# Kernel tuning notes

Hardware: AMD Instinct MI355X
Metric: run time of the kernel (lower is better)

Reference implementation:

```python
import jax, jax.numpy as jnp
import numpy as np

N = 50000   # num nodes
E = 800000  # num edges (avg degree 16)
L = 4       # num_blocks
H = 128     # hidden_dim
CD = 3      # coords_dim
VD = 3      # vel_dim
FD = 16     # node feature dim = node_dim - coords_dim - vel_dim
ED = 16     # edge_dim
DIN = 2 * H + ED + 1  # edge MLP input dim = 273


def setup_inputs() -> dict:
    key = jax.random.key(0)
    ks = jax.random.split(key, 32)
    s = 0.05
    inp = {}
    inp['nodes'] = jax.random.normal(ks[0], (N, CD + VD + FD), jnp.float32)
    # avoid self-loops (start==end) so the coord-diff norm is never exactly 0
    start = jax.random.randint(ks[1], (E,), 0, N)
    off = jax.random.randint(ks[2], (E,), 1, N)
    inp['edge_indices'] = jnp.stack([start, (start + off) % N]).astype(jnp.int64)
    inp['edge_features'] = jax.random.normal(ks[3], (E, ED), jnp.float32)
    # node embedding
    inp['emb_w'] = (jax.random.normal(ks[4], (FD, H)) * s).astype(jnp.float32)
    inp['emb_b'] = jnp.zeros((H,), jnp.float32)
    # per-block params, stacked over L blocks
    def w(k, shape):
        return (jax.random.normal(k, shape) * s).astype(jnp.float32)
    inp['ew1'] = w(ks[5], (L, DIN, H)); inp['eb1'] = jnp.zeros((L, H), jnp.float32)
    inp['ew2'] = w(ks[6], (L, H, H));   inp['eb2'] = jnp.zeros((L, H), jnp.float32)
    inp['cw1'] = w(ks[7], (L, H, H));   inp['cb1'] = jnp.zeros((L, H), jnp.float32)
    inp['cw2'] = w(ks[8], (L, H, CD));  inp['cb2'] = jnp.zeros((L, CD), jnp.float32)
    inp['vw1'] = w(ks[9], (L, H, H));   inp['vb1'] = jnp.zeros((L, H), jnp.float32)
    inp['vw2'] = w(ks[10], (L, H, 1));  inp['vb2'] = jnp.zeros((L, 1), jnp.float32)
    inp['nw1'] = w(ks[11], (L, 2 * H, H)); inp['nb1'] = jnp.zeros((L, H), jnp.float32)
    inp['nw2'] = w(ks[12], (L, H, H));  inp['nb2'] = jnp.zeros((L, H), jnp.float32)
    return inp


def _forward(nodes, edge_features, emb_w, emb_b, ew1, eb1, ew2, eb2,
             cw1, cb1, cw2, cb2, vw1, vb1, vw2, vb2, nw1, nb1, nw2, nb2,
             edge_indices):
    silu = jax.nn.silu
    coords = nodes[:, :CD]
    vels = nodes[:, CD:CD + VD]
    h = nodes[:, CD + VD:] @ emb_w + emb_b  # [N, H]
    start, end = edge_indices[0], edge_indices[1]
    n = coords.shape[0]
    # per-node edge counts for the coordinate mean-aggregation
    cnt = jax.ops.segment_sum(jnp.ones((start.shape[0], 1), coords.dtype),
                              start, num_segments=n)
    cnt = jnp.maximum(cnt, 1.0)
    for l in range(L):
        cd = coords[start] - coords[end]                       # [E, CD]
        nrm = jnp.sqrt(jnp.sum(cd * cd, axis=1, keepdims=True))  # [E, 1]
        x = jnp.concatenate([h[start], h[end], nrm, edge_features], axis=1)
        m = silu(silu(x @ ew1[l] + eb1[l]) @ ew2[l] + eb2[l])  # [E, H]
        # coordinate update: mean-aggregated weighted diffs + velocity term
        ct = cd * (silu(m @ cw1[l] + cb1[l]) @ cw2[l] + cb2[l])
        coords = coords + jax.ops.segment_sum(ct, start, num_segments=n) / cnt
        coords = coords + (silu(h @ vw1[l] + vb1[l]) @ vw2[l] + vb2[l]) * vels
        # node update: sum-aggregated messages
        agg = jax.ops.segment_sum(m, start, num_segments=n)    # [N, H]
        h = h + silu(jnp.concatenate([h, agg], axis=1) @ nw1[l] + nb1[l]) @ nw2[l] + nb2[l]
    return coords  # prediction_type == 'coords'


def reference(nodes, edge_indices, edge_features, emb_w, emb_b,
              ew1, eb1, ew2, eb2, cw1, cb1, cw2, cb2,
              vw1, vb1, vw2, vb2, nw1, nb1, nw2, nb2):
    return _forward(nodes, edge_features, emb_w, emb_b, ew1, eb1, ew2, eb2,
                    cw1, cb1, cw2, cb2, vw1, vb1, vw2, vb2,
                    nw1, nb1, nw2, nb2, edge_indices)
```

## Files before the change

### kernel.cpp

```cpp
#include <hip/hip_runtime.h>

constexpr int NN = 50000;
constexpr int EE = 800000;
constexpr int HH = 128;

typedef __attribute__((ext_vector_type(8))) __bf16 bfv8;
typedef __attribute__((ext_vector_type(4))) float f32x4;
typedef unsigned short u16;

__device__ __forceinline__ u16 f2bf(float x){
  unsigned u = __builtin_bit_cast(unsigned, x);
  u = u + 0x7fffu + ((u >> 16) & 1u);
  return (u16)(u >> 16);
}
__device__ __forceinline__ float fsilu(float x){
  return x * __builtin_amdgcn_rcpf(1.f + __expf(-x));
}

template<int KSTEPS, int CB>
__device__ __forceinline__ void mm_lds(const u16* Arows, const u16* __restrict__ Bp,
                                       const float* __restrict__ bias, int NB, f32x4* acc){
  const int lane = threadIdx.x & 63;
  #pragma unroll
  for (int cb = 0; cb < CB; ++cb){
    int col = cb*16 + (lane & 15);
    float b = (col < NB) ? bias[col] : 0.f;
    acc[cb] = (f32x4){b, b, b, b};
  }
  const int arow = lane & 15;
  const char* abase = (const char*)Arows + arow * 256;
  const int kb = (lane >> 4) * 16;
  const int swz = (arow & 7) << 4;
  const bfv8* __restrict__ bq = (const bfv8*)Bp + lane;
  #pragma unroll
  for (int ks = 0; ks < KSTEPS; ++ks){
    bfv8 a = *(const bfv8*)(abase + ((ks*64 + kb) ^ swz));
    #pragma unroll
    for (int cb = 0; cb < CB; ++cb)
      acc[cb] = __builtin_amdgcn_mfma_f32_16x16x32_bf16(a, bq[(ks*CB + cb) * 64], acc[cb], 0, 0, 0);
  }
}

template<int CB>
__device__ __forceinline__ void silu_store(const f32x4* acc, u16* dst){
  const int lane = threadIdx.x & 63;
  #pragma unroll
  for (int cb = 0; cb < CB; ++cb){
    #pragma unroll
    for (int j = 0; j < 4; ++j){
      int row = ((lane >> 4) << 2) + j;
      int col = cb*16 + (lane & 15);
      float s = fsilu(acc[cb][j]);
      *(u16*)((char*)dst + row*256 + ((col*2) ^ ((row & 7) << 4))) = f2bf(s);
    }
  }
}

struct PackDesc { const float* src; u16* dst; int K; int Nc; int CB; int ksteps; int remap; };
struct PackArgs { PackDesc d[32]; };

__global__ __launch_bounds__(256) void pack_kernel(PackArgs pa){
  PackDesc d = pa.d[blockIdx.x];
  int total = d.ksteps * d.CB * 512;
  for (int p = threadIdx.x; p < total; p += 256){
    int j = p & 7, lane = (p >> 3) & 63, cbk = p >> 9;
    int cb = cbk % d.CB, ks = cbk / d.CB;
    int k = ks*32 + ((lane >> 4) * 8) + j;
    int col = cb*16 + (lane & 15);
    int kk = k;
    if (d.remap && k >= 256) kk = (k < 272) ? (k + 1) : ((k == 272) ? 256 : 0x7fffffff);
    float v = (kk < d.K && col < d.Nc) ? d.src[(size_t)kk * d.Nc + col] : 0.f;
    d.dst[p] = f2bf(v);
  }
}

__global__ __launch_bounds__(256) void embed_kernel(const float* __restrict__ nodes,
    const float* __restrict__ emb_w, const float* __restrict__ emb_b,
    float* __restrict__ hf, u16* __restrict__ hbf, float* __restrict__ coords){
  int t = blockIdx.x * 256 + threadIdx.x;
  int g = t >> 2, q = t & 3;
  if (g >= NN) return;
  const float* x = nodes + (size_t)g * 22;
  float acc[32];
  #pragma unroll
  for (int c = 0; c < 32; ++c) acc[c] = emb_b[q*32 + c];
  for (int k = 0; k < 16; ++k){
    float f = x[6 + k];
    const float* wr = emb_w + k*128 + q*32;
    #pragma unroll
    for (int c = 0; c < 32; ++c) acc[c] += f * wr[c];
  }
  size_t off = (size_t)g * HH + q*32;
  #pragma unroll
  for (int c = 0; c < 32; ++c){ hf[off + c] = acc[c]; hbf[off + c] = f2bf(acc[c]); }
  if (q == 0){
    coords[g*3+0] = x[0]; coords[g*3+1] = x[1]; coords[g*3+2] = x[2];
  }
}

__global__ __launch_bounds__(256) void count_kernel(const int* __restrict__ esrc, int* __restrict__ cnt_i){
  int e = blockIdx.x * 256 + threadIdx.x;
  if (e < EE) atomicAdd(&cnt_i[esrc[e]], 1);
}

__global__ __launch_bounds__(256) void scan_kernel(const int* __restrict__ cnt_i,
    int* __restrict__ row_start, int* __restrict__ fill){
  __shared__ int part[256];
  int t = threadIdx.x;
  int lo = t * 196, hi = lo + 196;
  if (lo > NN) lo = NN;
  if (hi > NN) hi = NN;
  int s = 0;
  for (int i = lo; i < hi; ++i) s += cnt_i[i];
  part[t] = s; __syncthreads();
  for (int d = 1; d < 256; d <<= 1){
    int v = (t >= d) ? part[t-d] : 0;
    __syncthreads();
    part[t] += v;
    __syncthreads();
  }
  int run = part[t] - s;
  for (int i = lo; i < hi; ++i){ row_start[i] = run; fill[i] = run; run += cnt_i[i]; }
  if (t == 255) row_start[NN] = run;
}

__global__ __launch_bounds__(256) void scatter_kernel(const int* __restrict__ esrc,
    const int* __restrict__ edst, int* __restrict__ fill,
    int2* __restrict__ sd_sorted, int* __restrict__ eid_sorted){
  int e = blockIdx.x * 256 + threadIdx.x;
  if (e < EE){
    int s = esrc[e];
    int pos = atomicAdd(&fill[s], 1);
    sd_sorted[pos] = make_int2(s, edst[e]);
    eid_sorted[pos] = e;
  }
}

__global__ __launch_bounds__(256, 4) void edge_kernel(
    const float* __restrict__ coords, const u16* __restrict__ hbf, const float* __restrict__ ef,
    const int2* __restrict__ sd_sorted, const int* __restrict__ eid_sorted,
    const u16* __restrict__ ew1p, const u16* __restrict__ ew2p,
    const u16* __restrict__ cw1p, const u16* __restrict__ cw2p,
    const float* __restrict__ eb1, const float* __restrict__ eb2,
    const float* __restrict__ cb1, const float* __restrict__ cb2,
    float* __restrict__ agg, float* __restrict__ acc_ct){
  __shared__ __align__(16) u16 sBuf[4][2048];
  __shared__ float4 s_cdn[64];
  __shared__ int s_src[64];
  __shared__ int s_eid[64];

  const int tid = threadIdx.x, wid = tid >> 6, lane = tid & 63;
  const int R = wid * 16;
  const int e0 = blockIdx.x * 64;

  if (lane < 16){
    int row = R + lane;
    int e = e0 + row;
    int2 sd = sd_sorted[e];
    float cx = coords[sd.x*3+0] - coords[sd.y*3+0];
    float cy = coords[sd.x*3+1] - coords[sd.y*3+1];
    float cz = coords[sd.x*3+2] - coords[sd.y*3+2];
    float nrm = sqrtf(cx*cx + cy*cy + cz*cz);
    s_cdn[row] = make_float4(cx, cy, cz, nrm);
    s_src[row] = sd.x; s_eid[row] = eid_sorted[e];
  }
  {
    const int myrow = R + (lane & 15);
    const int g = lane >> 4;
    int e = e0 + myrow;
    int2 sd = sd_sorted[e];
    const u16* hsb = hbf + (size_t)sd.x * HH + g*8;
    const u16* hdb = hbf + (size_t)sd.y * HH + g*8;
    const int my_eid = s_eid[myrow];
    u16* sB = sBuf[wid];

    f32x4 acc[8];
    {
      const bfv8* __restrict__ bq = (const bfv8*)ew1p + lane;
      #pragma unroll
      for (int cb = 0; cb < 8; ++cb){
        float b = eb1[cb*16 + (lane & 15)];
        acc[cb] = (f32x4){b, b, b, b};
      }
      #pragma unroll
      for (int ks = 0; ks < 4; ++ks){
        bfv8 a = *(const bfv8*)(hsb + ks*32);
        #pragma unroll
        for (int cb = 0; cb < 8; ++cb)
          acc[cb] = __builtin_amdgcn_mfma_f32_16x16x32_bf16(a, bq[(ks*8 + cb)*64], acc[cb], 0, 0, 0);
      }
      #pragma unroll
      for (int ks = 4; ks < 8; ++ks){
        bfv8 a = *(const bfv8*)(hdb + (ks - 4)*32);
        #pragma unroll
        for (int cb = 0; cb < 8; ++cb)
          acc[cb] = __builtin_amdgcn_mfma_f32_16x16x32_bf16(a, bq[(ks*8 + cb)*64], acc[cb], 0, 0, 0);
      }
      union { bfv8 v; u16 s[8]; unsigned u[4]; } at;
      at.u[0] = at.u[1] = at.u[2] = at.u[3] = 0u;
      if (g < 2){
        float4 f0 = *(const float4*)(ef + (size_t)my_eid * 16 + g*8);
        float4 f1 = *(const float4*)(ef + (size_t)my_eid * 16 + g*8 + 4);
        at.u[0] = f2bf(f0.x) | ((unsigned)f2bf(f0.y) << 16);
        at.u[1] = f2bf(f0.z) | ((unsigned)f2bf(f0.w) << 16);
        at.u[2] = f2bf(f1.x) | ((unsigned)f2bf(f1.y) << 16);
        at.u[3] = f2bf(f1.z) | ((unsigned)f2bf(f1.w) << 16);
      } else if (g == 2){
        at.s[0] = f2bf(s_cdn[myrow].w);
      }
      #pragma unroll
      for (int cb = 0; cb < 8; ++cb)
        acc[cb] = __builtin_amdgcn_mfma_f32_16x16x32_bf16(at.v, bq[(8*8 + cb)*64], acc[cb], 0, 0, 0);
    }
    silu_store<8>(acc, sB);

    mm_lds<4, 8>(sB, ew2p, eb2, 128, acc);
    {
      const int rb = (lane >> 4) << 2;
      float run[8];
      #pragma unroll
      for (int cb = 0; cb < 8; ++cb) run[cb] = 0.f;
      #pragma unroll
      for (int j = 0; j < 4; ++j){
        int lrow = rb + j, grow = R + lrow;
        int src = s_src[grow];
        bool flush = (j == 3) || (s_src[grow + 1] != src);
        #pragma unroll
        for (int cb = 0; cb < 8; ++cb){
          int col = cb*16 + (lane & 15);
          float m = fsilu(acc[cb][j]);
          run[cb] += m;
          *(u16*)((char*)sB + lrow*256 + ((col*2) ^ ((lrow & 7) << 4))) = f2bf(m);
        }
        if (flush){
          #pragma unroll
          for (int cb = 0; cb < 8; ++cb){
            int col = cb*16 + (lane & 15);
            atomicAdd(&agg[(size_t)src * HH + col], run[cb]);
            run[cb] = 0.f;
          }
        }
      }
    }

    mm_lds<4, 8>(sB, cw1p, cb1, 128, acc);
    silu_store<8>(acc, sB);

    f32x4 a4[1];
    mm_lds<4, 1>(sB, cw2p, cb2, 3, a4);
    {
      int col = lane & 15;
      if (col < 3){
        const int rb = (lane >> 4) << 2;
        float run = 0.f;
        #pragma unroll
        for (int j = 0; j < 4; ++j){
          int grow = R + rb + j;
          float4 cdn = s_cdn[grow];
          float cdv = (col == 0) ? cdn.x : ((col == 1) ? cdn.y : cdn.z);
          run += cdv * a4[0][j];
          int src = s_src[grow];
          if (j == 3 || s_src[grow + 1] != src){
            atomicAdd(&acc_ct[(size_t)src * 3 + col], run);
            run = 0.f;
          }
        }
      }
    }
  }
}

__global__ __launch_bounds__(256, 4) void node_kernel(
    float* __restrict__ coords, float* __restrict__ hf, u16* __restrict__ hbf,
    const float* __restrict__ agg, const float* __restrict__ acc_ct, const int* __restrict__ row_start,
    const float* __restrict__ nodes,
    const u16* __restrict__ vw1p, const u16* __restrict__ vw2p,
    const u16* __restrict__ nw1p, const u16* __restrict__ nw2p,
    const float* __restrict__ vb1, const float* __restrict__ vb2,
    const float* __restrict__ nb1, const float* __restrict__ nb2){
  __shared__ __align__(16) u16 sV[4][2048];
  __shared__ float s_vt[64];

  const int tid = threadIdx.x, wid = tid >> 6, lane = tid & 63;
  const int R = wid * 16;
  const int g0 = blockIdx.x * 64;

  const int myrow = R + (lane & 15);
  const int gnode = g0 + myrow;
  const int arow = (gnode < NN) ? gnode : (NN - 1);
  const int g = lane >> 4;
  const u16*  hb = hbf + (size_t)arow * HH + g*8;
  const float* ab = agg + (size_t)arow * HH + g*8;

  f32x4 acc[8];
  {
    const bfv8* __restrict__ bq = (const bfv8*)vw1p + lane;
    #pragma unroll
    for (int cb = 0; cb < 8; ++cb){
      float b = vb1[cb*16 + (lane & 15)];
      acc[cb] = (f32x4){b, b, b, b};
    }
    #pragma unroll
    for (int ks = 0; ks < 4; ++ks){
      bfv8 a = *(const bfv8*)(hb + ks*32);
      #pragma unroll
      for (int cb = 0; cb < 8; ++cb)
        acc[cb] = __builtin_amdgcn_mfma_f32_16x16x32_bf16(a, bq[(ks*8 + cb)*64], acc[cb], 0, 0, 0);
    }
  }
  silu_store<8>(acc, sV[wid]);
  f32x4 a1[1];
  mm_lds<4, 1>(sV[wid], vw2p, vb2, 1, a1);
  if ((lane & 15) == 0){
    #pragma unroll
    for (int j = 0; j < 4; ++j) s_vt[R + ((lane >> 4) << 2) + j] = a1[0][j];
  }
  if (lane < 16){
    int row = R + lane, gg = g0 + row;
    if (gg < NN){
      float cn = (float)(row_start[gg + 1] - row_start[gg]);
      if (cn < 1.f) cn = 1.f;
      float vt = s_vt[row];
      #pragma unroll
      for (int c = 0; c < 3; ++c){
        float val = coords[gg*3 + c] + acc_ct[gg*3 + c] / cn + vt * nodes[(size_t)gg*22 + 3 + c];
        coords[gg*3 + c] = val;
      }
    }
  }

  {
    const bfv8* __restrict__ bq = (const bfv8*)nw1p + lane;
    #pragma unroll
    for (int cb = 0; cb < 8; ++cb){
      float b = nb1[cb*16 + (lane & 15)];
      acc[cb] = (f32x4){b, b, b, b};
    }
    #pragma unroll
    for (int ks = 0; ks < 4; ++ks){
      bfv8 a = *(const bfv8*)(hb + ks*32);
      #pragma unroll
      for (int cb = 0; cb < 8; ++cb)
        acc[cb] = __builtin_amdgcn_mfma_f32_16x16x32_bf16(a, bq[(ks*8 + cb)*64], acc[cb], 0, 0, 0);
    }
    #pragma unroll
    for (int ks = 4; ks < 8; ++ks){
      float4 f0 = *(const float4*)(ab + (ks - 4)*32);
      float4 f1 = *(const float4*)(ab + (ks - 4)*32 + 4);
      union { bfv8 v; unsigned u[4]; } aa;
      aa.u[0] = f2bf(f0.x) | ((unsigned)f2bf(f0.y) << 16);
      aa.u[1] = f2bf(f0.z) | ((unsigned)f2bf(f0.w) << 16);
      aa.u[2] = f2bf(f1.x) | ((unsigned)f2bf(f1.y) << 16);
      aa.u[3] = f2bf(f1.z) | ((unsigned)f2bf(f1.w) << 16);
      #pragma unroll
      for (int cb = 0; cb < 8; ++cb)
        acc[cb] = __builtin_amdgcn_mfma_f32_16x16x32_bf16(aa.v, bq[(ks*8 + cb)*64], acc[cb], 0, 0, 0);
    }
  }
  silu_store<8>(acc, sV[wid]);
  mm_lds<4, 8>(sV[wid], nw2p, nb2, 128, acc);
  {
    #pragma unroll
    for (int cb = 0; cb < 8; ++cb){
      int col = cb*16 + (lane & 15);
      #pragma unroll
      for (int j = 0; j < 4; ++j){
        int row = R + ((lane >> 4) << 2) + j, gg = g0 + row;
        if (gg < NN){
          size_t off = (size_t)gg * HH + col;
          float h = acc[cb][j] + hf[off];
          hf[off] = h;
          hbf[off] = f2bf(h);
        }
      }
    }
  }
}

extern "C" void kernel_launch(void* const* d_in, const int* in_sizes, int n_in,
                              void* d_out, int out_size, void* d_ws, size_t ws_size,
                              hipStream_t stream){
  const float* nodes = (const float*)d_in[0];
  const int*   eidx  = (const int*)d_in[1];
  const float* ef    = (const float*)d_in[2];
  const float* emb_w = (const float*)d_in[3];
  const float* emb_b = (const float*)d_in[4];
  const float* ew1 = (const float*)d_in[5];
  const float* eb1 = (const float*)d_in[6];
  const float* ew2 = (const float*)d_in[7];
  const float* eb2 = (const float*)d_in[8];
  const float* cw1 = (const float*)d_in[9];
  const float* cb1 = (const float*)d_in[10];
  const float* cw2 = (const float*)d_in[11];
  const float* cb2 = (const float*)d_in[12];
  const float* vw1 = (const float*)d_in[13];
  const float* vb1 = (const float*)d_in[14];
  const float* vw2 = (const float*)d_in[15];
  const float* vb2 = (const float*)d_in[16];
  const float* nw1 = (const float*)d_in[17];
  const float* nb1 = (const float*)d_in[18];
  const float* nw2 = (const float*)d_in[19];
  const float* nb2 = (const float*)d_in[20];

  constexpr size_t WS_NEEDED = 78u * 1024u * 1024u;
  if (ws_size < WS_NEEDED) return;

  char* ws = (char*)d_ws;
  size_t off = 0;
  auto alloc = [&](size_t bytes){ void* p = ws + off; off += (bytes + 255) & ~(size_t)255; return p; };
  float* coords   = (float*)alloc((size_t)NN * 3 * 4);
  float* hf       = (float*)alloc((size_t)NN * HH * 4);
  u16*   hbf      = (u16*)  alloc((size_t)NN * HH * 2);
  float* agg      = (float*)alloc((size_t)NN * 131 * 4);
  float* acc_ct   = agg + (size_t)NN * HH;
  int*   cnt_i    = (int*)  alloc((size_t)NN * 4);
  int*   row_start= (int*)  alloc((size_t)(NN + 1) * 4);
  int*   fill     = (int*)  alloc((size_t)NN * 4);
  int2*  sd_sorted= (int2*) alloc((size_t)EE * 8);
  int*   eid_sorted=(int*)  alloc((size_t)EE * 4);

  constexpr int O_EW1 = 0;
  constexpr int O_EW2 = O_EW1 + 9*8*512;
  constexpr int O_CW1 = O_EW2 + 4*8*512;
  constexpr int O_CW2 = O_CW1 + 4*8*512;
  constexpr int O_VW1 = O_CW2 + 4*1*512;
  constexpr int O_VW2 = O_VW1 + 4*8*512;
  constexpr int O_NW1 = O_VW2 + 4*1*512;
  constexpr int O_NW2 = O_NW1 + 8*8*512;
  constexpr int LAYER_PACK = O_NW2 + 4*8*512;
  u16* packs = (u16*)alloc((size_t)LAYER_PACK * 4 * 2);

  PackArgs pa;
  for (int l = 0; l < 4; ++l){
    u16* base = packs + (size_t)l * LAYER_PACK;
    int i = l * 8;
    pa.d[i+0] = { ew1 + (size_t)l*273*128, base + O_EW1, 273, 128, 8, 9, 1 };
    pa.d[i+1] = { ew2 + (size_t)l*128*128, base + O_EW2, 128, 128, 8, 4, 0 };
    pa.d[i+2] = { cw1 + (size_t)l*128*128, base + O_CW1, 128, 128, 8, 4, 0 };
    pa.d[i+3] = { cw2 + (size_t)l*128*3,   base + O_CW2, 128,   3, 1, 4, 0 };
    pa.d[i+4] = { vw1 + (size_t)l*128*128, base + O_VW1, 128, 128, 8, 4, 0 };
    pa.d[i+5] = { vw2 + (size_t)l*128*1,   base + O_VW2, 128,   1, 1, 4, 0 };
    pa.d[i+6] = { nw1 + (size_t)l*256*128, base + O_NW1, 256, 128, 8, 8, 0 };
    pa.d[i+7] = { nw2 + (size_t)l*128*128, base + O_NW2, 128, 128, 8, 4, 0 };
  }

  pack_kernel<<<32, 256, 0, stream>>>(pa);
  embed_kernel<<<(NN*4 + 255)/256, 256, 0, stream>>>(nodes, emb_w, emb_b, hf, hbf, coords);
  hipMemsetAsync(cnt_i, 0, (size_t)NN * 4, stream);
  count_kernel<<<(EE + 255)/256, 256, 0, stream>>>(eidx, cnt_i);
  scan_kernel<<<1, 256, 0, stream>>>(cnt_i, row_start, fill);
  scatter_kernel<<<(EE + 255)/256, 256, 0, stream>>>(eidx, eidx + EE, fill, sd_sorted, eid_sorted);

  for (int l = 0; l < 4; ++l){
    hipMemsetAsync(agg, 0, (size_t)NN * 131 * 4, stream);
    u16* base = packs + (size_t)l * LAYER_PACK;
    edge_kernel<<<EE/64, 256, 0, stream>>>(coords, hbf, ef, sd_sorted, eid_sorted,
        base + O_EW1, base + O_EW2, base + O_CW1, base + O_CW2,
        eb1 + l*128, eb2 + l*128, cb1 + l*128, cb2 + l*3, agg, acc_ct);
    node_kernel<<<(NN + 63)/64, 256, 0, stream>>>(coords, hf, hbf, agg, acc_ct, row_start, nodes,
        base + O_VW1, base + O_VW2, base + O_NW1, base + O_NW2,
        vb1 + l*128, vb2 + l, nb1 + l*128, nb2 + l*128);
  }

  hipMemcpyAsync(d_out, coords, (size_t)NN * 3 * 4, hipMemcpyDeviceToDevice, stream);
}
```

Before: 2.184 ms.

## Process two 16-edge MFMA tiles per wave in edge kernel to reuse weight fragments

Each wave in the edge kernel now handles 32 edges as two 16-row tiles. Every weight fragment loaded from global memory feeds two MFMAs instead of one, which halves weight traffic per edge, and the grid shrinks to EE/128 blocks. Shared buffers, the segment-sum flushes and the coord atomics are duplicated for the second tile, and the occupancy hint in launch_bounds is dropped. Doubling the accumulators raises register pressure and may lower occupancy. The node kernel is switched to new single-tile helpers with runtime-bound loops, which rely on constant propagation to avoid dynamic indexing of the accumulator array.

```diff
diff --git a/kernel.cpp b/kernel.cpp
--- a/kernel.cpp
+++ b/kernel.cpp
@@ -18,31 +18,39 @@
 }
 
 template<int KSTEPS, int CB>
-__device__ __forceinline__ void mm_lds(const u16* Arows, const u16* __restrict__ Bp,
-                                       const float* __restrict__ bias, int NB, f32x4* acc){
+__device__ __forceinline__ void mm_lds2(const u16* tile, const u16* __restrict__ Bp,
+                                        const float* __restrict__ bias, int NB,
+                                        f32x4* acc0, f32x4* acc1){
   const int lane = threadIdx.x & 63;
   #pragma unroll
   for (int cb = 0; cb < CB; ++cb){
     int col = cb*16 + (lane & 15);
     float b = (col < NB) ? bias[col] : 0.f;
-    acc[cb] = (f32x4){b, b, b, b};
+    acc0[cb] = (f32x4){b, b, b, b};
+    acc1[cb] = (f32x4){b, b, b, b};
   }
   const int arow = lane & 15;
-  const char* abase = (const char*)Arows + arow * 256;
+  const char* abase0 = (const char*)tile + arow * 256;
+  const char* abase1 = abase0 + 16 * 256;
   const int kb = (lane >> 4) * 16;
   const int swz = (arow & 7) << 4;
   const bfv8* __restrict__ bq = (const bfv8*)Bp + lane;
   #pragma unroll
   for (int ks = 0; ks < KSTEPS; ++ks){
-    bfv8 a = *(const bfv8*)(abase + ((ks*64 + kb) ^ swz));
-    #pragma unroll
-    for (int cb = 0; cb < CB; ++cb)
-      acc[cb] = __builtin_amdgcn_mfma_f32_16x16x32_bf16(a, bq[(ks*CB + cb) * 64], acc[cb], 0, 0, 0);
+    int off = (ks*64 + kb) ^ swz;
+    bfv8 a0 = *(const bfv8*)(abase0 + off);
+    bfv8 a1 = *(const bfv8*)(abase1 + off);
+    #pragma unroll
+    for (int cb = 0; cb < CB; ++cb){
+      bfv8 b = bq[(ks*CB + cb) * 64];
+      acc0[cb] = __builtin_amdgcn_mfma_f32_16x16x32_bf16(a0, b, acc0[cb], 0, 0, 0);
+      acc1[cb] = __builtin_amdgcn_mfma_f32_16x16x32_bf16(a1, b, acc1[cb], 0, 0, 0);
+    }
   }
 }
 
 template<int CB>
-__device__ __forceinline__ void silu_store(const f32x4* acc, u16* dst){
+__device__ __forceinline__ void silu_store2(const f32x4* acc0, const f32x4* acc1, u16* dst){
   const int lane = threadIdx.x & 63;
   #pragma unroll
   for (int cb = 0; cb < CB; ++cb){
@@ -50,8 +58,9 @@
     for (int j = 0; j < 4; ++j){
       int row = ((lane >> 4) << 2) + j;
       int col = cb*16 + (lane & 15);
-      float s = fsilu(acc[cb][j]);
-      *(u16*)((char*)dst + row*256 + ((col*2) ^ ((row & 7) << 4))) = f2bf(s);
+      int sw = ((col*2) ^ ((row & 7) << 4));
+      *(u16*)((char*)dst + row*256 + sw)        = f2bf(fsilu(acc0[cb][j]));
+      *(u16*)((char*)dst + (row+16)*256 + sw)   = f2bf(fsilu(acc1[cb][j]));
     }
   }
 }
@@ -136,7 +145,7 @@
   }
 }
 
-__global__ __launch_bounds__(256, 4) void edge_kernel(
+__global__ __launch_bounds__(256) void edge_kernel(
     const float* __restrict__ coords, const u16* __restrict__ hbf, const float* __restrict__ ef,
     const int2* __restrict__ sd_sorted, const int* __restrict__ eid_sorted,
     const u16* __restrict__ ew1p, const u16* __restrict__ ew2p,
@@ -144,16 +153,16 @@
     const float* __restrict__ eb1, const float* __restrict__ eb2,
     const float* __restrict__ cb1, const float* __restrict__ cb2,
     float* __restrict__ agg, float* __restrict__ acc_ct){
-  __shared__ __align__(16) u16 sBuf[4][2048];
-  __shared__ float4 s_cdn[64];
-  __shared__ int s_src[64];
-  __shared__ int s_eid[64];
+  __shared__ __align__(16) u16 sBuf[4][4096];
+  __shared__ float4 s_cdn[128];
+  __shared__ int s_src[128];
+  __shared__ int s_eid[128];
 
   const int tid = threadIdx.x, wid = tid >> 6, lane = tid & 63;
-  const int R = wid * 16;
-  const int e0 = blockIdx.x * 64;
-
-  if (lane < 16){
+  const int R = wid * 32;
+  const int e0 = blockIdx.x * 128;
+
+  if (lane < 32){
     int row = R + lane;
     int e = e0 + row;
     int2 sd = sd_sorted[e];
@@ -165,56 +174,79 @@
     s_src[row] = sd.x; s_eid[row] = eid_sorted[e];
   }
   {
-    const int myrow = R + (lane & 15);
+    const int r0 = R + (lane & 15), r1 = r0 + 16;
     const int g = lane >> 4;
-    int e = e0 + myrow;
-    int2 sd = sd_sorted[e];
-    const u16* hsb = hbf + (size_t)sd.x * HH + g*8;
-    const u16* hdb = hbf + (size_t)sd.y * HH + g*8;
-    const int my_eid = s_eid[myrow];
+    int2 sd0 = sd_sorted[e0 + r0];
+    int2 sd1 = sd_sorted[e0 + r1];
+    const u16* hsb0 = hbf + (size_t)sd0.x * HH + g*8;
+    const u16* hdb0 = hbf + (size_t)sd0.y * HH + g*8;
+    const u16* hsb1 = hbf + (size_t)sd1.x * HH + g*8;
+    const u16* hdb1 = hbf + (size_t)sd1.y * HH + g*8;
+    const int eid0 = s_eid[r0], eid1 = s_eid[r1];
     u16* sB = sBuf[wid];
 
-    f32x4 acc[8];
+    f32x4 acc0[8], acc1[8];
     {
       const bfv8* __restrict__ bq = (const bfv8*)ew1p + lane;
       #pragma unroll
       for (int cb = 0; cb < 8; ++cb){
         float b = eb1[cb*16 + (lane & 15)];
-        acc[cb] = (f32x4){b, b, b, b};
+        acc0[cb] = (f32x4){b, b, b, b};
+        acc1[cb] = (f32x4){b, b, b, b};
       }
       #pragma unroll
       for (int ks = 0; ks < 4; ++ks){
-        bfv8 a = *(const bfv8*)(hsb + ks*32);
+        bfv8 a0 = *(const bfv8*)(hsb0 + ks*32);
+        bfv8 a1 = *(const bfv8*)(hsb1 + ks*32);
         #pragma unroll
-        for (int cb = 0; cb < 8; ++cb)
-          acc[cb] = __builtin_amdgcn_mfma_f32_16x16x32_bf16(a, bq[(ks*8 + cb)*64], acc[cb], 0, 0, 0);
+        for (int cb = 0; cb < 8; ++cb){
+          bfv8 b = bq[(ks*8 + cb)*64];
+          acc0[cb] = __builtin_amdgcn_mfma_f32_16x16x32_bf16(a0, b, acc0[cb], 0, 0, 0);
+          acc1[cb] = __builtin_amdgcn_mfma_f32_16x16x32_bf16(a1, b, acc1[cb], 0, 0, 0);
+        }
       }
       #pragma unroll
       for (int ks = 4; ks < 8; ++ks){
-        bfv8 a = *(const bfv8*)(hdb + (ks - 4)*32);
+        bfv8 a0 = *(const bfv8*)(hdb0 + (ks - 4)*32);
+        bfv8 a1 = *(const bfv8*)(hdb1 + (ks - 4)*32);
         #pragma unroll
-        for (int cb = 0; cb < 8; ++cb)
-          acc[cb] = __builtin_amdgcn_mfma_f32_16x16x32_bf16(a, bq[(ks*8 + cb)*64], acc[cb], 0, 0, 0);
-      }
-      union { bfv8 v; u16 s[8]; unsigned u[4]; } at;
-      at.u[0] = at.u[1] = at.u[2] = at.u[3] = 0u;
+        for (int cb = 0; cb < 8; ++cb){
+          bfv8 b = bq[(ks*8 + cb)*64];
+          acc0[cb] = __builtin_amdgcn_mfma_f32_16x16x32_bf16(a0, b, acc0[cb], 0, 0, 0);
+          acc1[cb] = __builtin_amdgcn_mfma_f32_16x16x32_bf16(a1, b, acc1[cb], 0, 0, 0);
+        }
+      }
+      union U { bfv8 v; u16 s[8]; unsigned u[4]; };
+      U at0, at1;
+      at0.u[0]=at0.u[1]=at0.u[2]=at0.u[3]=0u;
+      at1.u[0]=at1.u[1]=at1.u[2]=at1.u[3]=0u;
       if (g < 2){
-        float4 f0 = *(const float4*)(ef + (size_t)my_eid * 16 + g*8);
-        float4 f1 = *(const float4*)(ef + (size_t)my_eid * 16 + g*8 + 4);
-        at.u[0] = f2bf(f0.x) | ((unsigned)f2bf(f0.y) << 16);
-        at.u[1] = f2bf(f0.z) | ((unsigned)f2bf(f0.w) << 16);
-        at.u[2] = f2bf(f1.x) | ((unsigned)f2bf(f1.y) << 16);
-        at.u[3] = f2bf(f1.z) | ((unsigned)f2bf(f1.w) << 16);
+        float4 f0 = *(const float4*)(ef + (size_t)eid0 * 16 + g*8);
+        float4 f1 = *(const float4*)(ef + (size_t)eid0 * 16 + g*8 + 4);
+        at0.u[0] = f2bf(f0.x) | ((unsigned)f2bf(f0.y) << 16);
+        at0.u[1] = f2bf(f0.z) | ((unsigned)f2bf(f0.w) << 16);
+        at0.u[2] = f2bf(f1.x) | ((unsigned)f2bf(f1.y) << 16);
+        at0.u[3] = f2bf(f1.z) | ((unsigned)f2bf(f1.w) << 16);
+        float4 g0v = *(const float4*)(ef + (size_t)eid1 * 16 + g*8);
+        float4 g1v = *(const float4*)(ef + (size_t)eid1 * 16 + g*8 + 4);
+        at1.u[0] = f2bf(g0v.x) | ((unsigned)f2bf(g0v.y) << 16);
+        at1.u[1] = f2bf(g0v.z) | ((unsigned)f2bf(g0v.w) << 16);
+        at1.u[2] = f2bf(g1v.x) | ((unsigned)f2bf(g1v.y) << 16);
+        at1.u[3] = f2bf(g1v.z) | ((unsigned)f2bf(g1v.w) << 16);
       } else if (g == 2){
-        at.s[0] = f2bf(s_cdn[myrow].w);
-      }
-      #pragma unroll
-      for (int cb = 0; cb < 8; ++cb)
-        acc[cb] = __builtin_amdgcn_mfma_f32_16x16x32_bf16(at.v, bq[(8*8 + cb)*64], acc[cb], 0, 0, 0);
-    }
-    silu_store<8>(acc, sB);
-
-    mm_lds<4, 8>(sB, ew2p, eb2, 128, acc);
+        at0.s[0] = f2bf(s_cdn[r0].w);
+        at1.s[0] = f2bf(s_cdn[r1].w);
+      }
+      #pragma unroll
+      for (int cb = 0; cb < 8; ++cb){
+        bfv8 b = bq[(8*8 + cb)*64];
+        acc0[cb] = __builtin_amdgcn_mfma_f32_16x16x32_bf16(at0.v, b, acc0[cb], 0, 0, 0);
+        acc1[cb] = __builtin_amdgcn_mfma_f32_16x16x32_bf16(at1.v, b, acc1[cb], 0, 0, 0);
+      }
+    }
+    silu_store2<8>(acc0, acc1, sB);
+
+    mm_lds2<4, 8>(sB, ew2p, eb2, 128, acc0, acc1);
     {
       const int rb = (lane >> 4) << 2;
       float run[8];
@@ -228,7 +260,7 @@
         #pragma unroll
         for (int cb = 0; cb < 8; ++cb){
           int col = cb*16 + (lane & 15);
-          float m = fsilu(acc[cb][j]);
+          float m = fsilu(acc0[cb][j]);
           run[cb] += m;
           *(u16*)((char*)sB + lrow*256 + ((col*2) ^ ((lrow & 7) << 4))) = f2bf(m);
         }
@@ -241,13 +273,36 @@
           }
         }
       }
-    }
-
-    mm_lds<4, 8>(sB, cw1p, cb1, 128, acc);
-    silu_store<8>(acc, sB);
-
-    f32x4 a4[1];
-    mm_lds<4, 1>(sB, cw2p, cb2, 3, a4);
+      #pragma unroll
+      for (int cb = 0; cb < 8; ++cb) run[cb] = 0.f;
+      #pragma unroll
+      for (int j = 0; j < 4; ++j){
+        int lrow = 16 + rb + j, grow = R + lrow;
+        int src = s_src[grow];
+        bool flush = (j == 3) || (s_src[grow + 1] != src);
+        #pragma unroll
+        for (int cb = 0; cb < 8; ++cb){
+          int col = cb*16 + (lane & 15);
+          float m = fsilu(acc1[cb][j]);
+          run[cb] += m;
+          *(u16*)((char*)sB + lrow*256 + ((col*2) ^ ((lrow & 7) << 4))) = f2bf(m);
+        }
+        if (flush){
+          #pragma unroll
+          for (int cb = 0; cb < 8; ++cb){
+            int col = cb*16 + (lane & 15);
+            atomicAdd(&agg[(size_t)src * HH + col], run[cb]);
+            run[cb] = 0.f;
+          }
+        }
+      }
+    }
+
+    mm_lds2<4, 8>(sB, cw1p, cb1, 128, acc0, acc1);
+    silu_store2<8>(acc0, acc1, sB);
+
+    f32x4 a40[1], a41[1];
+    mm_lds2<4, 1>(sB, cw2p, cb2, 3, a40, a41);
     {
       int col = lane & 15;
       if (col < 3){
@@ -258,15 +313,49 @@
           int grow = R + rb + j;
           float4 cdn = s_cdn[grow];
           float cdv = (col == 0) ? cdn.x : ((col == 1) ? cdn.y : cdn.z);
-          run += cdv * a4[0][j];
+          run += cdv * a40[0][j];
           int src = s_src[grow];
           if (j == 3 || s_src[grow + 1] != src){
             atomicAdd(&acc_ct[(size_t)src * 3 + col], run);
             run = 0.f;
           }
         }
-      }
-    }
+        run = 0.f;
+        #pragma unroll
+        for (int j = 0; j < 4; ++j){
+          int grow = R + 16 + rb + j;
+          float4 cdn = s_cdn[grow];
+          float cdv = (col == 0) ? cdn.x : ((col == 1) ? cdn.y : cdn.z);
+          run += cdv * a41[0][j];
+          int src = s_src[grow];
+          if (j == 3 || s_src[grow + 1] != src){
+            atomicAdd(&acc_ct[(size_t)src * 3 + col], run);
+            run = 0.f;
+          }
+        }
+      }
+    }
+  }
+}
+
+__device__ __forceinline__ void mm_lds1(const u16* Arows, const u16* __restrict__ Bp,
+                                        const float* __restrict__ bias, int NB, int CBn,
+                                        int KS, f32x4* acc){
+  const int lane = threadIdx.x & 63;
+  for (int cb = 0; cb < CBn; ++cb){
+    int col = cb*16 + (lane & 15);
+    float b = (col < NB) ? bias[col] : 0.f;
+    acc[cb] = (f32x4){b, b, b, b};
+  }
+  const int arow = lane & 15;
+  const char* abase = (const char*)Arows + arow * 256;
+  const int kb = (lane >> 4) * 16;
+  const int swz = (arow & 7) << 4;
+  const bfv8* __restrict__ bq = (const bfv8*)Bp + lane;
+  for (int ks = 0; ks < KS; ++ks){
+    bfv8 a = *(const bfv8*)(abase + ((ks*64 + kb) ^ swz));
+    for (int cb = 0; cb < CBn; ++cb)
+      acc[cb] = __builtin_amdgcn_mfma_f32_16x16x32_bf16(a, bq[(ks*CBn + cb) * 64], acc[cb], 0, 0, 0);
   }
 }
 
@@ -308,9 +397,19 @@
         acc[cb] = __builtin_amdgcn_mfma_f32_16x16x32_bf16(a, bq[(ks*8 + cb)*64], acc[cb], 0, 0, 0);
     }
   }
-  silu_store<8>(acc, sV[wid]);
+  {
+    #pragma unroll
+    for (int cb = 0; cb < 8; ++cb){
+      #pragma unroll
+      for (int j = 0; j < 4; ++j){
+        int row = ((lane >> 4) << 2) + j;
+        int col = cb*16 + (lane & 15);
+        *(u16*)((char*)sV[wid] + row*256 + ((col*2) ^ ((row & 7) << 4))) = f2bf(fsilu(acc[cb][j]));
+      }
+    }
+  }
   f32x4 a1[1];
-  mm_lds<4, 1>(sV[wid], vw2p, vb2, 1, a1);
+  mm_lds1(sV[wid], vw2p, vb2, 1, 1, 4, a1);
   if ((lane & 15) == 0){
     #pragma unroll
     for (int j = 0; j < 4; ++j) s_vt[R + ((lane >> 4) << 2) + j] = a1[0][j];
@@ -357,8 +456,18 @@
         acc[cb] = __builtin_amdgcn_mfma_f32_16x16x32_bf16(aa.v, bq[(ks*8 + cb)*64], acc[cb], 0, 0, 0);
     }
   }
-  silu_store<8>(acc, sV[wid]);
-  mm_lds<4, 8>(sV[wid], nw2p, nb2, 128, acc);
+  {
+    #pragma unroll
+    for (int cb = 0; cb < 8; ++cb){
+      #pragma unroll
+      for (int j = 0; j < 4; ++j){
+        int row = ((lane >> 4) << 2) + j;
+        int col = cb*16 + (lane & 15);
+        *(u16*)((char*)sV[wid] + row*256 + ((col*2) ^ ((row & 7) << 4))) = f2bf(fsilu(acc[cb][j]));
+      }
+    }
+  }
+  mm_lds1(sV[wid], nw2p, nb2, 128, 8, 4, acc);
   {
     #pragma unroll
     for (int cb = 0; cb < 8; ++cb){
@@ -454,7 +563,7 @@
   for (int l = 0; l < 4; ++l){
     hipMemsetAsync(agg, 0, (size_t)NN * 131 * 4, stream);
     u16* base = packs + (size_t)l * LAYER_PACK;
-    edge_kernel<<<EE/64, 256, 0, stream>>>(coords, hbf, ef, sd_sorted, eid_sorted,
+    edge_kernel<<<EE/128, 256, 0, stream>>>(coords, hbf, ef, sd_sorted, eid_sorted,
         base + O_EW1, base + O_EW2, base + O_CW1, base + O_CW2,
         eb1 + l*128, eb2 + l*128, cb1 + l*128, cb2 + l*3, agg, acc_ct);
     node_kernel<<<(NN + 63)/64, 256, 0, stream>>>(coords, hf, hbf, agg, acc_ct, row_start, nodes,
```

New measurement: 2.279 ms. 4.4% more time.

## Stage edge-MLP weight tiles through shared memory with block-wide syncs

Applied to the files above, without the earlier changes.

The edge kernel now copies each packed weight matrix (ew1 in three chunks, then ew2, cw1, cw2) into a 32KB shared-memory buffer cooperatively before each matmul, so MFMA B operands are read from LDS instead of global or L2. This adds many __syncthreads barriers and raises LDS use per block, and the launch-bounds occupancy hint is dropped. The node kernel switches to a non-unrolled generic matmul helper with runtime loop counts, which may hurt codegen there. The intent is to cut repeated global weight traffic, at the cost of lower occupancy and serialized copy phases.

```diff
diff --git a/kernel.cpp b/kernel.cpp
--- a/kernel.cpp
+++ b/kernel.cpp
@@ -17,9 +17,15 @@
   return x * __builtin_amdgcn_rcpf(1.f + __expf(-x));
 }
 
+__device__ __forceinline__ void stagecpy(u16* __restrict__ dst, const u16* __restrict__ src, int n16){
+  const uint4* s = (const uint4*)src;
+  uint4* d = (uint4*)dst;
+  for (int i = threadIdx.x; i < n16; i += 256) d[i] = s[i];
+}
+
 template<int KSTEPS, int CB>
-__device__ __forceinline__ void mm_lds(const u16* Arows, const u16* __restrict__ Bp,
-                                       const float* __restrict__ bias, int NB, f32x4* acc){
+__device__ __forceinline__ void mmW(const u16* Arows, const u16* __restrict__ Bstage,
+                                    const float* __restrict__ bias, int NB, f32x4* acc){
   const int lane = threadIdx.x & 63;
   #pragma unroll
   for (int cb = 0; cb < CB; ++cb){
@@ -31,7 +37,7 @@
   const char* abase = (const char*)Arows + arow * 256;
   const int kb = (lane >> 4) * 16;
   const int swz = (arow & 7) << 4;
-  const bfv8* __restrict__ bq = (const bfv8*)Bp + lane;
+  const bfv8* bq = (const bfv8*)Bstage + lane;
   #pragma unroll
   for (int ks = 0; ks < KSTEPS; ++ks){
     bfv8 a = *(const bfv8*)(abase + ((ks*64 + kb) ^ swz));
@@ -50,8 +56,7 @@
     for (int j = 0; j < 4; ++j){
       int row = ((lane >> 4) << 2) + j;
       int col = cb*16 + (lane & 15);
-      float s = fsilu(acc[cb][j]);
-      *(u16*)((char*)dst + row*256 + ((col*2) ^ ((row & 7) << 4))) = f2bf(s);
+      *(u16*)((char*)dst + row*256 + ((col*2) ^ ((row & 7) << 4))) = f2bf(fsilu(acc[cb][j]));
     }
   }
 }
@@ -136,7 +141,7 @@
   }
 }
 
-__global__ __launch_bounds__(256, 4) void edge_kernel(
+__global__ __launch_bounds__(256) void edge_kernel(
     const float* __restrict__ coords, const u16* __restrict__ hbf, const float* __restrict__ ef,
     const int2* __restrict__ sd_sorted, const int* __restrict__ eid_sorted,
     const u16* __restrict__ ew1p, const u16* __restrict__ ew2p,
@@ -144,6 +149,7 @@
     const float* __restrict__ eb1, const float* __restrict__ eb2,
     const float* __restrict__ cb1, const float* __restrict__ cb2,
     float* __restrict__ agg, float* __restrict__ acc_ct){
+  __shared__ __align__(16) u16 sStage[16384];
   __shared__ __align__(16) u16 sBuf[4][2048];
   __shared__ float4 s_cdn[64];
   __shared__ int s_src[64];
@@ -152,6 +158,8 @@
   const int tid = threadIdx.x, wid = tid >> 6, lane = tid & 63;
   const int R = wid * 16;
   const int e0 = blockIdx.x * 64;
+
+  stagecpy(sStage, ew1p, 2048);
 
   if (lane < 16){
     int row = R + lane;
@@ -164,109 +172,148 @@
     s_cdn[row] = make_float4(cx, cy, cz, nrm);
     s_src[row] = sd.x; s_eid[row] = eid_sorted[e];
   }
-  {
-    const int myrow = R + (lane & 15);
-    const int g = lane >> 4;
-    int e = e0 + myrow;
-    int2 sd = sd_sorted[e];
-    const u16* hsb = hbf + (size_t)sd.x * HH + g*8;
-    const u16* hdb = hbf + (size_t)sd.y * HH + g*8;
+
+  const int myrow = R + (lane & 15);
+  const int g = lane >> 4;
+  int2 sd = sd_sorted[e0 + myrow];
+  const u16* hsb = hbf + (size_t)sd.x * HH + g*8;
+  const u16* hdb = hbf + (size_t)sd.y * HH + g*8;
+  u16* sB = sBuf[wid];
+  const bfv8* bqs = (const bfv8*)sStage + lane;
+
+  f32x4 acc[8];
+  __syncthreads();
+  {
+    #pragma unroll
+    for (int cb = 0; cb < 8; ++cb){
+      float b = eb1[cb*16 + (lane & 15)];
+      acc[cb] = (f32x4){b, b, b, b};
+    }
+    #pragma unroll
+    for (int ks = 0; ks < 4; ++ks){
+      bfv8 a = *(const bfv8*)(hsb + ks*32);
+      #pragma unroll
+      for (int cb = 0; cb < 8; ++cb)
+        acc[cb] = __builtin_amdgcn_mfma_f32_16x16x32_bf16(a, bqs[(ks*8 + cb)*64], acc[cb], 0, 0, 0);
+    }
+  }
+  __syncthreads();
+  stagecpy(sStage, ew1p + 4*8*512, 2048);
+  __syncthreads();
+  {
+    #pragma unroll
+    for (int ks = 0; ks < 4; ++ks){
+      bfv8 a = *(const bfv8*)(hdb + ks*32);
+      #pragma unroll
+      for (int cb = 0; cb < 8; ++cb)
+        acc[cb] = __builtin_amdgcn_mfma_f32_16x16x32_bf16(a, bqs[(ks*8 + cb)*64], acc[cb], 0, 0, 0);
+    }
+  }
+  __syncthreads();
+  stagecpy(sStage, ew1p + 8*8*512, 512);
+  __syncthreads();
+  {
     const int my_eid = s_eid[myrow];
-    u16* sB = sBuf[wid];
-
-    f32x4 acc[8];
-    {
-      const bfv8* __restrict__ bq = (const bfv8*)ew1p + lane;
+    union { bfv8 v; u16 s[8]; unsigned u[4]; } at;
+    at.u[0] = at.u[1] = at.u[2] = at.u[3] = 0u;
+    if (g < 2){
+      float4 f0 = *(const float4*)(ef + (size_t)my_eid * 16 + g*8);
+      float4 f1 = *(const float4*)(ef + (size_t)my_eid * 16 + g*8 + 4);
+      at.u[0] = f2bf(f0.x) | ((unsigned)f2bf(f0.y) << 16);
+      at.u[1] = f2bf(f0.z) | ((unsigned)f2bf(f0.w) << 16);
+      at.u[2] = f2bf(f1.x) | ((unsigned)f2bf(f1.y) << 16);
+      at.u[3] = f2bf(f1.z) | ((unsigned)f2bf(f1.w) << 16);
+    } else if (g == 2){
+      at.s[0] = f2bf(s_cdn[myrow].w);
+    }
+    #pragma unroll
+    for (int cb = 0; cb < 8; ++cb)
+      acc[cb] = __builtin_amdgcn_mfma_f32_16x16x32_bf16(at.v, bqs[cb*64], acc[cb], 0, 0, 0);
+  }
+  silu_store<8>(acc, sB);
+
+  __syncthreads();
+  stagecpy(sStage, ew2p, 2048);
+  __syncthreads();
+  mmW<4, 8>(sB, sStage, eb2, 128, acc);
+  {
+    const int rb = (lane >> 4) << 2;
+    float run[8];
+    #pragma unroll
+    for (int cb = 0; cb < 8; ++cb) run[cb] = 0.f;
+    #pragma unroll
+    for (int j = 0; j < 4; ++j){
+      int lrow = rb + j, grow = R + lrow;
+      int src = s_src[grow];
+      bool flush = (j == 3) || (s_src[grow + 1] != src);
       #pragma unroll
       for (int cb = 0; cb < 8; ++cb){
-        float b = eb1[cb*16 + (lane & 15)];
-        acc[cb] = (f32x4){b, b, b, b};
-      }
-      #pragma unroll
-      for (int ks = 0; ks < 4; ++ks){
-        bfv8 a = *(const bfv8*)(hsb + ks*32);
-        #pragma unroll
-        for (int cb = 0; cb < 8; ++cb)
-          acc[cb] = __builtin_amdgcn_mfma_f32_16x16x32_bf16(a, bq[(ks*8 + cb)*64], acc[cb], 0, 0, 0);
-      }
-      #pragma unroll
-      for (int ks = 4; ks < 8; ++ks){
-        bfv8 a = *(const bfv8*)(hdb + (ks - 4)*32);
-        #pragma unroll
-        for (int cb = 0; cb < 8; ++cb)
-          acc[cb] = __builtin_amdgcn_mfma_f32_16x16x32_bf16(a, bq[(ks*8 + cb)*64], acc[cb], 0, 0, 0);
-      }
-      union { bfv8 v; u16 s[8]; unsigned u[4]; } at;
-      at.u[0] = at.u[1] = at.u[2] = at.u[3] = 0u;
-      if (g < 2){
-        float4 f0 = *(const float4*)(ef + (size_t)my_eid * 16 + g*8);
-        float4 f1 = *(const float4*)(ef + (size_t)my_eid * 16 + g*8 + 4);
-        at.u[0] = f2bf(f0.x) | ((unsigned)f2bf(f0.y) << 16);
-        at.u[1] = f2bf(f0.z) | ((unsigned)f2bf(f0.w) << 16);
-        at.u[2] = f2bf(f1.x) | ((unsigned)f2bf(f1.y) << 16);
-        at.u[3] = f2bf(f1.z) | ((unsigned)f2bf(f1.w) << 16);
-      } else if (g == 2){
-        at.s[0] = f2bf(s_cdn[myrow].w);
-      }
-      #pragma unroll
-      for (int cb = 0; cb < 8; ++cb)
-        acc[cb] = __builtin_amdgcn_mfma_f32_16x16x32_bf16(at.v, bq[(8*8 + cb)*64], acc[cb], 0, 0, 0);
-    }
-    silu_store<8>(acc, sB);
-
-    mm_lds<4, 8>(sB, ew2p, eb2, 128, acc);
-    {
-      const int rb = (lane >> 4) << 2;
-      float run[8];
-      #pragma unroll
-      for (int cb = 0; cb < 8; ++cb) run[cb] = 0.f;
-      #pragma unroll
-      for (int j = 0; j < 4; ++j){
-        int lrow = rb + j, grow = R + lrow;
-        int src = s_src[grow];
-        bool flush = (j == 3) || (s_src[grow + 1] != src);
+        int col = cb*16 + (lane & 15);
+        float m = fsilu(acc[cb][j]);
+        run[cb] += m;
+        *(u16*)((char*)sB + lrow*256 + ((col*2) ^ ((lrow & 7) << 4))) = f2bf(m);
+      }
+      if (flush){
         #pragma unroll
         for (int cb = 0; cb < 8; ++cb){
           int col = cb*16 + (lane & 15);
-          float m = fsilu(acc[cb][j]);
-          run[cb] += m;
-          *(u16*)((char*)sB + lrow*256 + ((col*2) ^ ((lrow & 7) << 4))) = f2bf(m);
+          atomicAdd(&agg[(size_t)src * HH + col], run[cb]);
+          run[cb] = 0.f;
         }
-        if (flush){
-          #pragma unroll
-          for (int cb = 0; cb < 8; ++cb){
-            int col = cb*16 + (lane & 15);
-            atomicAdd(&agg[(size_t)src * HH + col], run[cb]);
-            run[cb] = 0.f;
-          }
+      }
+    }
+  }
+
+  __syncthreads();
+  stagecpy(sStage, cw1p, 2048);
+  __syncthreads();
+  mmW<4, 8>(sB, sStage, cb1, 128, acc);
+  silu_store<8>(acc, sB);
+
+  __syncthreads();
+  stagecpy(sStage, cw2p, 256);
+  __syncthreads();
+  f32x4 a4[1];
+  mmW<4, 1>(sB, sStage, cb2, 3, a4);
+  {
+    int col = lane & 15;
+    if (col < 3){
+      const int rb = (lane >> 4) << 2;
+      float run = 0.f;
+      #pragma unroll
+      for (int j = 0; j < 4; ++j){
+        int grow = R + rb + j;
+        float4 cdn = s_cdn[grow];
+        float cdv = (col == 0) ? cdn.x : ((col == 1) ? cdn.y : cdn.z);
+        run += cdv * a4[0][j];
+        int src = s_src[grow];
+        if (j == 3 || s_src[grow + 1] != src){
+          atomicAdd(&acc_ct[(size_t)src * 3 + col], run);
+          run = 0.f;
         }
       }
     }
-
-    mm_lds<4, 8>(sB, cw1p, cb1, 128, acc);
-    silu_store<8>(acc, sB);
-
-    f32x4 a4[1];
-    mm_lds<4, 1>(sB, cw2p, cb2, 3, a4);
-    {
-      int col = lane & 15;
-      if (col < 3){
-        const int rb = (lane >> 4) << 2;
-        float run = 0.f;
-        #pragma unroll
-        for (int j = 0; j < 4; ++j){
-          int grow = R + rb + j;
-          float4 cdn = s_cdn[grow];
-          float cdv = (col == 0) ? cdn.x : ((col == 1) ? cdn.y : cdn.z);
-          run += cdv * a4[0][j];
-          int src = s_src[grow];
-          if (j == 3 || s_src[grow + 1] != src){
-            atomicAdd(&acc_ct[(size_t)src * 3 + col], run);
-            run = 0.f;
-          }
-        }
-      }
-    }
+  }
+}
+
+__device__ __forceinline__ void mm_lds1(const u16* Arows, const u16* __restrict__ Bp,
+                                        const float* __restrict__ bias, int NB, int CBn,
+                                        int KS, f32x4* acc){
+  const int lane = threadIdx.x & 63;
+  for (int cb = 0; cb < CBn; ++cb){
+    int col = cb*16 + (lane & 15);
+    float b = (col < NB) ? bias[col] : 0.f;
+    acc[cb] = (f32x4){b, b, b, b};
+  }
+  const int arow = lane & 15;
+  const char* abase = (const char*)Arows + arow * 256;
+  const int kb = (lane >> 4) * 16;
+  const int swz = (arow & 7) << 4;
+  const bfv8* __restrict__ bq = (const bfv8*)Bp + lane;
+  for (int ks = 0; ks < KS; ++ks){
+    bfv8 a = *(const bfv8*)(abase + ((ks*64 + kb) ^ swz));
+    for (int cb = 0; cb < CBn; ++cb)
+      acc[cb] = __builtin_amdgcn_mfma_f32_16x16x32_bf16(a, bq[(ks*CBn + cb) * 64], acc[cb], 0, 0, 0);
   }
 }
 
@@ -308,9 +355,19 @@
         acc[cb] = __builtin_amdgcn_mfma_f32_16x16x32_bf16(a, bq[(ks*8 + cb)*64], acc[cb], 0, 0, 0);
     }
   }
-  silu_store<8>(acc, sV[wid]);
+  {
+    #pragma unroll
+    for (int cb = 0; cb < 8; ++cb){
+      #pragma unroll
+      for (int j = 0; j < 4; ++j){
+        int row = ((lane >> 4) << 2) + j;
+        int col = cb*16 + (lane & 15);
+        *(u16*)((char*)sV[wid] + row*256 + ((col*2) ^ ((row & 7) << 4))) = f2bf(fsilu(acc[cb][j]));
+      }
+    }
+  }
   f32x4 a1[1];
-  mm_lds<4, 1>(sV[wid], vw2p, vb2, 1, a1);
+  mm_lds1(sV[wid], vw2p, vb2, 1, 1, 4, a1);
   if ((lane & 15) == 0){
     #pragma unroll
     for (int j = 0; j < 4; ++j) s_vt[R + ((lane >> 4) << 2) + j] = a1[0][j];
@@ -357,8 +414,18 @@
         acc[cb] = __builtin_amdgcn_mfma_f32_16x16x32_bf16(aa.v, bq[(ks*8 + cb)*64], acc[cb], 0, 0, 0);
     }
   }
-  silu_store<8>(acc, sV[wid]);
-  mm_lds<4, 8>(sV[wid], nw2p, nb2, 128, acc);
+  {
+    #pragma unroll
+    for (int cb = 0; cb < 8; ++cb){
+      #pragma unroll
+      for (int j = 0; j < 4; ++j){
+        int row = ((lane >> 4) << 2) + j;
+        int col = cb*16 + (lane & 15);
+        *(u16*)((char*)sV[wid] + row*256 + ((col*2) ^ ((row & 7) << 4))) = f2bf(fsilu(acc[cb][j]));
+      }
+    }
+  }
+  mm_lds1(sV[wid], nw2p, nb2, 128, 8, 4, acc);
   {
     #pragma unroll
     for (int cb = 0; cb < 8; ++cb){
```

Result: faster. 2.096 ms (-4.0%).
